# Kernel optimization log

Hardware: AMD Instinct MI355X
Metric: run time of the kernel (lower is better)

## Reference

```python
import jax, jax.numpy as jnp
import numpy as np

IN_F, OUT_F = 2048, 2048
IQ, OQ = IN_F // 4, OUT_F // 4
B, S = 4, 4096


def _xavier(key, shape):
    fan_out, fan_in = shape
    limit = float(np.sqrt(6.0 / (fan_in + fan_out)))
    return jax.random.uniform(key, shape, jnp.float32, -limit, limit)


def setup_inputs() -> dict:
    key = jax.random.key(0)
    kx, kr, ki, kj, kk = jax.random.split(key, 5)
    return {
        "x": jax.random.normal(kx, (B, S, IN_F), dtype=jnp.float32),
        "wr": _xavier(kr, (OQ, IQ)),
        "wi": _xavier(ki, (OQ, IQ)),
        "wj": _xavier(kj, (OQ, IQ)),
        "wk": _xavier(kk, (OQ, IQ)),
        "bias": jnp.zeros((OUT_F,), dtype=jnp.float32),
    }


def reference(x, wr, wi, wj, wk, bias):
    b, s, _ = x.shape
    iq = wr.shape[1]
    oq = wr.shape[0]
    # strided quaternion component extraction: x[..., c::4] -> (B*S, iq)
    xq = x.reshape(b * s, iq, 4)  # last-dim interleaved layout
    xr, xi, xj, xk = xq[..., 0], xq[..., 1], xq[..., 2], xq[..., 3]
    # small GEMMs against W^T (W is (oq, iq)); only the products actually used
    Ar = xr @ wr.T
    Br = xi @ wr.T
    Cr = xj @ wr.T
    Dr = xk @ wr.T
    Ai = xr @ wi.T
    Bi = xi @ wi.T
    Aj = xr @ wj.T
    Cj = xj @ wj.T
    Ak = xr @ wk.T
    Dk = xk @ wk.T
    # combine exactly as in the original module
    or_ = Ar - Bi - Cj - Dk
    oi_ = Br + Ai + Dk - Cj
    oj_ = Cr - Dk + Aj + Bi
    ok_ = Dr + Cj - Bi + Ak
    # interleaved scatter: out[:, c::4] = o<c>
    out = jnp.stack([or_, oi_, oj_, ok_], axis=-1).reshape(b, s, 4 * oq)
    return out + bias[None, None, :]
```

## Files before the change

### kernel.cpp

```cpp
#include <hip/hip_runtime.h>


typedef unsigned short u16;
typedef __bf16 bf16x8 __attribute__((ext_vector_type(8)));
typedef float f32x4 __attribute__((ext_vector_type(4)));

#define QM 16384
#define QN 2048
#define QK 2048

__device__ __forceinline__ u16 f2bf(float f) {
    union { float f; unsigned u; } v;
    v.f = f;
    unsigned r = v.u + 0x7FFFu + ((v.u >> 16) & 1u);
    return (u16)(r >> 16);
}

__device__ __forceinline__ void async_copy16(const u16* g, u16* l) {
    __builtin_amdgcn_global_load_lds(
        (const __attribute__((address_space(1))) void*)g,
        (__attribute__((address_space(3))) void*)l,
        16, 0, 0);
}

__global__ void cvt_x_kernel(const float* __restrict__ x, u16* __restrict__ y, int n4) {
    for (int i = blockIdx.x * blockDim.x + threadIdx.x; i < n4; i += gridDim.x * blockDim.x) {
        float4 v = reinterpret_cast<const float4*>(x)[i];
        ushort4 o;
        o.x = f2bf(v.x); o.y = f2bf(v.y); o.z = f2bf(v.z); o.w = f2bf(v.w);
        reinterpret_cast<ushort4*>(y)[i] = o;
    }
}

__global__ void pack_w_kernel(const float* __restrict__ wr, const float* __restrict__ wi,
                              const float* __restrict__ wj, const float* __restrict__ wk,
                              u16* __restrict__ W) {
    int i = blockIdx.x * blockDim.x + threadIdx.x;
    if (i >= QN * (QK / 4)) return;
    int n = i >> 9;
    int p = i & 511;
    int q = n >> 2, co = n & 3;
    int base = (q << 9) + p;
    float r  = wr[base], ii = wi[base], jj = wj[base], kk = wk[base];
    float e0, e1, e2, e3;
    if      (co == 0) { e0 = r;  e1 = -ii; e2 = -jj; e3 = -kk; }
    else if (co == 1) { e0 = ii; e1 = r;   e2 = -jj; e3 = kk;  }
    else if (co == 2) { e0 = jj; e1 = ii;  e2 = r;   e3 = -kk; }
    else              { e0 = kk; e1 = -ii; e2 = jj;  e3 = r;   }
    ushort4 o;
    o.x = f2bf(e0); o.y = f2bf(e1); o.z = f2bf(e2); o.w = f2bf(e3);
    reinterpret_cast<ushort4*>(W)[(n << 9) + p] = o;
}

__global__ __launch_bounds__(512, 2) void qgemm_kernel(const u16* __restrict__ A,
                                                       const u16* __restrict__ B,
                                                       const float* __restrict__ bias,
                                                       float* __restrict__ C) {
    __shared__ __align__(16) u16 L[2 * 32768];

    const int bid = blockIdx.x;
    const int swz = (bid & 7) * 64 + (bid >> 3);
    const int bm = swz >> 3;
    const int bn = swz & 7;

    const int tid = threadIdx.x;
    const int wid = tid >> 6, lane = tid & 63;
    const int wm = wid >> 2, wn = wid & 3;
    const int lr = lane & 15, lg = lane >> 4;

    const u16* Asrc = A + (size_t)bm * 256 * QK;
    const u16* Bsrc = B + (size_t)bn * 256 * QK;

    const int rA  = tid >> 3;
    const int clA = ((tid & 7) ^ (rA & 7)) << 3;
    const size_t soff = (size_t)rA * QK + clA;

    f32x4 acc[8][4];
#pragma unroll
    for (int i = 0; i < 8; ++i)
#pragma unroll
        for (int j = 0; j < 4; ++j)
            acc[i][j] = (f32x4){0.f, 0.f, 0.f, 0.f};

    auto stage = [&](const u16* src, int lbase, int k0) {
#pragma unroll
        for (int o = 0; o < 2; ++o)
            async_copy16(src + (size_t)(o * 64) * QK + k0 + soff,
                         &L[lbase + o * 4096 + wid * 512]);
    };

    auto rdA = [&](const u16* LA, int mf, int ks) -> bf16x8 {
        const int r = wm * 128 + mf * 16 + lr;
        const int c = ((ks * 4 + lg) ^ (r & 7)) << 3;
        return *(const bf16x8*)&LA[r * 64 + c];
    };
    auto rdB = [&](const u16* LB, int nf, int ks) -> bf16x8 {
        const int r = wn * 64 + nf * 16 + lr;
        const int c = ((ks * 4 + lg) ^ (r & 7)) << 3;
        return *(const bf16x8*)&LB[r * 64 + c];
    };

    auto doTile = [&](const int b, const int t) __attribute__((always_inline)) {
        const u16* LA = &L[b * 32768];
        const u16* LB = LA + 16384;
        const int tw1 = (t + 1) & 31, tw2 = (t + 2) & 31;
        const int ob = (b ^ 1) * 32768;
        const int cb = b * 32768;

        bf16x8 a0[4], a1[4], b0[4], b1[4];

#pragma unroll
        for (int nf = 0; nf < 4; ++nf) b0[nf] = rdB(LB, nf, 0);
#pragma unroll
        for (int mf = 0; mf < 4; ++mf) a0[mf] = rdA(LA, mf, 0);
        stage(Asrc, ob, tw1 * 64);
        __builtin_amdgcn_s_setprio(1);
#pragma unroll
        for (int mf = 0; mf < 4; ++mf)
#pragma unroll
            for (int nf = 0; nf < 4; ++nf)
                acc[mf][nf] = __builtin_amdgcn_mfma_f32_16x16x32_bf16(a0[mf], b0[nf], acc[mf][nf], 0, 0, 0);
        __builtin_amdgcn_s_setprio(0);
#pragma unroll
        for (int mf = 0; mf < 4; ++mf) a1[mf] = rdA(LA, 4 + mf, 0);
#pragma unroll
        for (int nf = 0; nf < 4; ++nf) b1[nf] = rdB(LB, nf, 1);
        stage(Asrc + 128 * QK, ob + 8192, tw1 * 64);
        __builtin_amdgcn_s_setprio(1);
#pragma unroll
        for (int mf = 0; mf < 4; ++mf)
#pragma unroll
            for (int nf = 0; nf < 4; ++nf)
                acc[4 + mf][nf] = __builtin_amdgcn_mfma_f32_16x16x32_bf16(a1[mf], b0[nf], acc[4 + mf][nf], 0, 0, 0);
        __builtin_amdgcn_s_setprio(0);

        asm volatile("s_waitcnt lgkmcnt(0)" ::: "memory");
        __builtin_amdgcn_s_barrier();

#pragma unroll
        for (int mf = 0; mf < 4; ++mf) a0[mf] = rdA(LA, mf, 1);
        stage(Bsrc, cb + 16384, tw2 * 64);
        __builtin_amdgcn_s_setprio(1);
#pragma unroll
        for (int mf = 0; mf < 4; ++mf)
#pragma unroll
            for (int nf = 0; nf < 4; ++nf)
                acc[mf][nf] = __builtin_amdgcn_mfma_f32_16x16x32_bf16(a0[mf], b1[nf], acc[mf][nf], 0, 0, 0);
        __builtin_amdgcn_s_setprio(0);
#pragma unroll
        for (int mf = 0; mf < 4; ++mf) a1[mf] = rdA(LA, 4 + mf, 1);
        stage(Bsrc + 128 * QK, cb + 16384 + 8192, tw2 * 64);
        __builtin_amdgcn_s_setprio(1);
#pragma unroll
        for (int mf = 0; mf < 4; ++mf)
#pragma unroll
            for (int nf = 0; nf < 4; ++nf)
                acc[4 + mf][nf] = __builtin_amdgcn_mfma_f32_16x16x32_bf16(a1[mf], b1[nf], acc[4 + mf][nf], 0, 0, 0);
        __builtin_amdgcn_s_setprio(0);

        asm volatile("s_waitcnt lgkmcnt(0) vmcnt(4)" ::: "memory");
        __builtin_amdgcn_s_barrier();
    };

    stage(Asrc,            0,                 0);
    stage(Asrc + 128 * QK, 8192,              0);
    stage(Bsrc,            16384,             0);
    stage(Bsrc + 128 * QK, 16384 + 8192,      0);
    stage(Bsrc,            32768 + 16384,        64);
    stage(Bsrc + 128 * QK, 32768 + 16384 + 8192, 64);
    asm volatile("s_waitcnt vmcnt(4)" ::: "memory");
    __builtin_amdgcn_s_barrier();

    for (int t = 0; t < 32; t += 2) {
        doTile(0, t);
        doTile(1, t + 1);
    }

    const int colbase = bn * 256 + wn * 64;
    const int rowbase = bm * 256 + wm * 128;
    float bsv[4];
#pragma unroll
    for (int nf = 0; nf < 4; ++nf) bsv[nf] = bias[colbase + nf * 16 + lr];
    float* Cb = C + (size_t)rowbase * QN + colbase;
#pragma unroll
    for (int mf = 0; mf < 8; ++mf)
#pragma unroll
        for (int nf = 0; nf < 4; ++nf)
#pragma unroll
            for (int v = 0; v < 4; ++v)
                Cb[(size_t)(mf * 16 + lg * 4 + v) * QN + nf * 16 + lr] = acc[mf][nf][v] + bsv[nf];
}

extern "C" void kernel_launch(void* const* d_in, const int* in_sizes, int n_in,
                              void* d_out, int out_size, void* d_ws, size_t ws_size,
                              hipStream_t stream) {
    const float* x    = (const float*)d_in[0];
    const float* wr   = (const float*)d_in[1];
    const float* wi   = (const float*)d_in[2];
    const float* wj   = (const float*)d_in[3];
    const float* wk   = (const float*)d_in[4];
    const float* bias = (const float*)d_in[5];
    float* out = (float*)d_out;

    u16* xb = (u16*)d_ws;
    u16* wb = (u16*)((char*)d_ws + (size_t)QM * QK * 2);

    cvt_x_kernel<<<4096, 256, 0, stream>>>(x, xb, (QM * QK) / 4);
    pack_w_kernel<<<4096, 256, 0, stream>>>(wr, wi, wj, wk, wb);
    qgemm_kernel<<<512, 512, 0, stream>>>(xb, wb, bias, out);
}
```

Measured before the change: 162.5 us.

## Triple-buffer B tiles in LDS to drop the mid-tile barrier

The kernel now allocates separate LDS regions, a double buffer for A and a rotating triple buffer for B, instead of two combined A+B buffers. With B prefetches going to a third slot, the mid-tile lgkmcnt wait and workgroup barrier are removed, leaving one barrier per K-step. LDS use per block grows from 128 KB to 160 KB. That can cut occupancy below the two blocks per CU the launch bounds target, and the loop is no longer unrolled by two with constant buffer indices.

```diff
diff --git a/kernel.cpp b/kernel.cpp
--- a/kernel.cpp
+++ b/kernel.cpp
@@ -56,7 +56,7 @@
                                                        const u16* __restrict__ B,
                                                        const float* __restrict__ bias,
                                                        float* __restrict__ C) {
-    __shared__ __align__(16) u16 L[2 * 32768];
+    __shared__ __align__(16) u16 L[81920];
 
     const int bid = blockIdx.x;
     const int swz = (bid & 7) * 64 + (bid >> 3);
@@ -100,12 +100,13 @@
         return *(const bf16x8*)&LB[r * 64 + c];
     };
 
-    auto doTile = [&](const int b, const int t) __attribute__((always_inline)) {
-        const u16* LA = &L[b * 32768];
-        const u16* LB = LA + 16384;
+    auto doTile = [&](const int ab, const int bt, const int bt2, const int t)
+        __attribute__((always_inline)) {
+        const u16* LA = &L[ab * 16384];
+        const u16* LB = &L[32768 + bt * 16384];
         const int tw1 = (t + 1) & 31, tw2 = (t + 2) & 31;
-        const int ob = (b ^ 1) * 32768;
-        const int cb = b * 32768;
+        const int oA = (ab ^ 1) * 16384;
+        const int oB = 32768 + bt2 * 16384;
 
         bf16x8 a0[4], a1[4], b0[4], b1[4];
 
@@ -113,7 +114,7 @@
         for (int nf = 0; nf < 4; ++nf) b0[nf] = rdB(LB, nf, 0);
 #pragma unroll
         for (int mf = 0; mf < 4; ++mf) a0[mf] = rdA(LA, mf, 0);
-        stage(Asrc, ob, tw1 * 64);
+        stage(Asrc, oA, tw1 * 64);
         __builtin_amdgcn_s_setprio(1);
 #pragma unroll
         for (int mf = 0; mf < 4; ++mf)
@@ -121,11 +122,12 @@
             for (int nf = 0; nf < 4; ++nf)
                 acc[mf][nf] = __builtin_amdgcn_mfma_f32_16x16x32_bf16(a0[mf], b0[nf], acc[mf][nf], 0, 0, 0);
         __builtin_amdgcn_s_setprio(0);
+
 #pragma unroll
         for (int mf = 0; mf < 4; ++mf) a1[mf] = rdA(LA, 4 + mf, 0);
 #pragma unroll
         for (int nf = 0; nf < 4; ++nf) b1[nf] = rdB(LB, nf, 1);
-        stage(Asrc + 128 * QK, ob + 8192, tw1 * 64);
+        stage(Asrc + 128 * QK, oA + 8192, tw1 * 64);
         __builtin_amdgcn_s_setprio(1);
 #pragma unroll
         for (int mf = 0; mf < 4; ++mf)
@@ -134,12 +136,9 @@
                 acc[4 + mf][nf] = __builtin_amdgcn_mfma_f32_16x16x32_bf16(a1[mf], b0[nf], acc[4 + mf][nf], 0, 0, 0);
         __builtin_amdgcn_s_setprio(0);
 
-        asm volatile("s_waitcnt lgkmcnt(0)" ::: "memory");
-        __builtin_amdgcn_s_barrier();
-
 #pragma unroll
         for (int mf = 0; mf < 4; ++mf) a0[mf] = rdA(LA, mf, 1);
-        stage(Bsrc, cb + 16384, tw2 * 64);
+        stage(Bsrc, oB, tw2 * 64);
         __builtin_amdgcn_s_setprio(1);
 #pragma unroll
         for (int mf = 0; mf < 4; ++mf)
@@ -147,9 +146,10 @@
             for (int nf = 0; nf < 4; ++nf)
                 acc[mf][nf] = __builtin_amdgcn_mfma_f32_16x16x32_bf16(a0[mf], b1[nf], acc[mf][nf], 0, 0, 0);
         __builtin_amdgcn_s_setprio(0);
+
 #pragma unroll
         for (int mf = 0; mf < 4; ++mf) a1[mf] = rdA(LA, 4 + mf, 1);
-        stage(Bsrc + 128 * QK, cb + 16384 + 8192, tw2 * 64);
+        stage(Bsrc + 128 * QK, oB + 8192, tw2 * 64);
         __builtin_amdgcn_s_setprio(1);
 #pragma unroll
         for (int mf = 0; mf < 4; ++mf)
@@ -162,18 +162,22 @@
         __builtin_amdgcn_s_barrier();
     };
 
-    stage(Asrc,            0,                 0);
-    stage(Asrc + 128 * QK, 8192,              0);
-    stage(Bsrc,            16384,             0);
-    stage(Bsrc + 128 * QK, 16384 + 8192,      0);
+    stage(Asrc,            0,             0);
+    stage(Asrc + 128 * QK, 8192,          0);
+    stage(Bsrc,            32768,             0);
+    stage(Bsrc + 128 * QK, 32768 + 8192,      0);
     stage(Bsrc,            32768 + 16384,        64);
     stage(Bsrc + 128 * QK, 32768 + 16384 + 8192, 64);
     asm volatile("s_waitcnt vmcnt(4)" ::: "memory");
     __builtin_amdgcn_s_barrier();
 
-    for (int t = 0; t < 32; t += 2) {
-        doTile(0, t);
-        doTile(1, t + 1);
+    {
+        int bt = 0, bt2 = 2;
+        for (int t = 0; t < 32; ++t) {
+            doTile(t & 1, bt, bt2, t);
+            bt  = (bt  == 2) ? 0 : bt  + 1;
+            bt2 = (bt2 == 2) ? 0 : bt2 + 1;
+        }
     }
 
     const int colbase = bn * 256 + wn * 64;
```

New measurement: 163.1 us. Within noise of the previous version (+0.4%).
